# Performance work log

Hardware: AMD Instinct MI355X
Metric: run time of the kernel (lower is better)

The kernel has to match this reference:

```python
import jax, jax.numpy as jnp
import numpy as np

OUT_H, OUT_W = 14, 14
SPATIAL_SCALE = 0.25

def setup_inputs() -> dict:
    key = jax.random.key(0)
    k1, k2, k3, k4, k5, k6 = jax.random.split(key, 6)
    B, C, H, W = 2, 256, 200, 336
    R = 1000
    features = jax.random.normal(k1, (B, C, H, W), jnp.float32)
    img_h, img_w = H / SPATIAL_SCALE, W / SPATIAL_SCALE
    cx = jax.random.uniform(k2, (R,)) * img_w
    cy = jax.random.uniform(k3, (R,)) * img_h
    bw = jax.random.uniform(k4, (R,)) * 256.0 + 16.0
    bh = jax.random.uniform(k5, (R,)) * 256.0 + 16.0
    x1 = jnp.clip(cx - bw / 2, 0.0, img_w - 1.0)
    x2 = jnp.clip(cx + bw / 2, 0.0, img_w - 1.0)
    y1 = jnp.clip(cy - bh / 2, 0.0, img_h - 1.0)
    y2 = jnp.clip(cy + bh / 2, 0.0, img_h - 1.0)
    bidx = jax.random.randint(k6, (R,), 0, B).astype(jnp.float32)
    rois = jnp.stack([bidx, x1, y1, x2, y2], axis=1)  # (R, 5)
    return {"features": features, "rois": rois}

def _roi_align(features, rois):
    # features: (B, C, H, W); rois: (R, 5) = (batch_idx, x1, y1, x2, y2) in image coords
    B, C, H, W = features.shape
    R = rois.shape[0]
    b = jax.lax.stop_gradient(rois[:, 0]).astype(jnp.int32)
    x1, y1, x2, y2 = rois[:, 1], rois[:, 2], rois[:, 3], rois[:, 4]
    # bin-center grid in [0,1] (affine_grid identity, align_corners=False, then normalized)
    gx = (jnp.arange(OUT_W, dtype=features.dtype) + 0.5) / OUT_W
    gy = (jnp.arange(OUT_H, dtype=features.dtype) + 0.5) / OUT_H
    px = x1[:, None] + gx[None, :] * (x2 - x1)[:, None]  # (R, OUT_W) abs image x
    py = y1[:, None] + gy[None, :] * (y2 - y1)[:, None]  # (R, OUT_H) abs image y
    # grid_sample(align_corners=False) with normalized coord abs/(size/scale): pix = abs*scale - 0.5
    fx = jnp.broadcast_to(px[:, None, :], (R, OUT_H, OUT_W)) * SPATIAL_SCALE - 0.5
    fy = jnp.broadcast_to(py[:, :, None], (R, OUT_H, OUT_W)) * SPATIAL_SCALE - 0.5
    x0 = jnp.floor(fx); y0 = jnp.floor(fy)
    lx = fx - x0; ly = fy - y0
    x0i = x0.astype(jnp.int32); y0i = y0.astype(jnp.int32)
    feats_flat = features.reshape(B, C, H * W)
    bb = b[:, None, None]  # (R,1,1)
    def corner(yi, xi):
        valid = ((xi >= 0) & (xi < W) & (yi >= 0) & (yi < H)).astype(features.dtype)
        idx = jnp.clip(yi, 0, H - 1) * W + jnp.clip(xi, 0, W - 1)  # (R,OUT_H,OUT_W)
        v = feats_flat[bb, :, idx]  # (R, OUT_H, OUT_W, C)
        return v * valid[..., None]  # zeros padding_mode
    v00 = corner(y0i, x0i)
    v01 = corner(y0i, x0i + 1)
    v10 = corner(y0i + 1, x0i)
    v11 = corner(y0i + 1, x0i + 1)
    wx0 = (1.0 - lx)[..., None]; wx1 = lx[..., None]
    wy0 = (1.0 - ly)[..., None]; wy1 = ly[..., None]
    out = wy0 * (wx0 * v00 + wx1 * v01) + wy1 * (wx0 * v10 + wx1 * v11)
    return out.transpose(0, 3, 1, 2)  # (R, C, OUT_H, OUT_W)

def reference(features, rois):
    return _roi_align(features, rois)
```

## Files before the change

kernel.cpp:

```cpp
#include <hip/hip_runtime.h>

constexpr int B = 2, C = 256, H = 200, W = 336;
constexpr int HW = H * W;
constexpr int OH = 14, OW = 14, OHW = OH * OW;
constexpr float SCALE = 0.25f;
constexpr int R = 1000;

constexpr int CSPLIT = 16;
constexpr int CPB = C / CSPLIT;
constexpr int NXCD = 8;
constexpr int RPX = R / NXCD;

constexpr int ITEMS = CPB * OHW;

constexpr int NYB = 13;
constexpr int NXB = 21;

typedef float f2 __attribute__((ext_vector_type(2), aligned(4)));

__global__ __launch_bounds__(1024) void bucket_rois_kernel(
    const float* __restrict__ rois, int* __restrict__ order)
{
    __shared__ int cnt[1024];
    const int t = threadIdx.x;
    cnt[t] = 0;
    __syncthreads();

    int k = 0, pos = 0;
    if (t < R) {
        const float* roi = rois + t * 5;
        const int   b  = (int)roi[0];
        const float cx = 0.5f * (roi[1] + roi[3]);
        const float cy = 0.5f * (roi[2] + roi[4]);
        const int yb = min(NYB - 1, max(0, (int)cy >> 6));
        const int xb = min(NXB - 1, max(0, (int)cx >> 6));
        k = (b * NYB + yb) * NXB + xb;
        pos = atomicAdd(&cnt[k], 1);
    }
    __syncthreads();

    for (int off = 1; off < 1024; off <<= 1) {
        const int add = (t >= off) ? cnt[t - off] : 0;
        __syncthreads();
        cnt[t] += add;
        __syncthreads();
    }

    if (t < R) {
        const int base = (k > 0) ? cnt[k - 1] : 0;
        order[base + pos] = t;
    }
}

__global__ __launch_bounds__(256, 8) void roi_align_kernel(
    const float* __restrict__ feat,
    const float* __restrict__ rois,
    const int*  __restrict__ order,
    float* __restrict__ out)
{
    __shared__ int   si0[OHW], si1[OHW];
    __shared__ float sa0[OHW], sb0[OHW], sa1[OHW], sb1[OHW];

    const int bid   = blockIdx.x;
    const int xcd   = bid & (NXCD - 1);
    const int slot  = bid >> 3;
    const int slice = slot & (CSPLIT - 1);
    const int rank  = slot >> 4;
    const int r     = __builtin_amdgcn_readfirstlane(order[xcd * RPX + rank]);
    const int c0    = slice * CPB;
    const int tid   = threadIdx.x;

    const float* roi = rois + r * 5;
    const float x1 = roi[1], y1 = roi[2], x2 = roi[3], y2 = roi[4];
    const int b = __builtin_amdgcn_readfirstlane((int)roi[0]);

    if (tid < OHW) {
        const int oh = tid / OW;
        const int ow = tid - oh * OW;

        const float fx = (x1 + (ow + 0.5f) * (1.0f / OW) * (x2 - x1)) * SCALE - 0.5f;
        const float fy = (y1 + (oh + 0.5f) * (1.0f / OH) * (y2 - y1)) * SCALE - 0.5f;

        const float x0f = floorf(fx), y0f = floorf(fy);
        const float lx = fx - x0f,   ly = fy - y0f;
        const int x0 = (int)x0f,  y0 = (int)y0f;
        const int x1i = x0 + 1,   y1i = y0 + 1;

        const float cxw0 = ((x0  >= 0 && x0  < W) ? 1.0f : 0.0f) * (1.0f - lx);
        const float cxw1 = ((x1i >= 0 && x1i < W) ? 1.0f : 0.0f) * lx;
        const float ryw0 = ((y0  >= 0 && y0  < H) ? 1.0f : 0.0f) * (1.0f - ly);
        const float ryw1 = ((y1i >= 0 && y1i < H) ? 1.0f : 0.0f) * ly;

        const int px = min(max(x0, 0), W - 2);
        const bool swp = (x0 != px);
        const float wxa = swp ? cxw1 : cxw0;
        const float wxb = swp ? cxw0 : cxw1;

        const int cy0 = min(max(y0,  0), H - 1);
        const int cy1 = min(max(y1i, 0), H - 1);

        si0[tid] = cy0 * W + px;
        si1[tid] = cy1 * W + px;
        sa0[tid] = ryw0 * wxa;
        sb0[tid] = ryw0 * wxb;
        sa1[tid] = ryw1 * wxa;
        sb1[tid] = ryw1 * wxb;
    }
    __syncthreads();

    const float* p  = feat + (size_t)(b * C + c0) * HW;
    float*       ob = out  + ((size_t)r * C + c0) * OHW;

    int idx = tid;
    #pragma unroll 1
    for (int bb = 0; bb < 3; ++bb) {
        const float* pa[4];
        const float* pb[4];
        float wa0[4], wb0[4], wa1[4], wb1[4];
        f2 v0[4], v1[4];

        #pragma unroll
        for (int u = 0; u < 4; ++u) {
            const int id = idx + u * 256;
            const int c  = id / OHW;
            const int s  = id - c * OHW;
            const int cb = c * HW;
            pa[u] = p + cb + si0[s];
            pb[u] = p + cb + si1[s];
            wa0[u] = sa0[s]; wb0[u] = sb0[s];
            wa1[u] = sa1[s]; wb1[u] = sb1[s];
        }
        #pragma unroll
        for (int u = 0; u < 4; ++u) {
            v0[u] = *reinterpret_cast<const f2*>(pa[u]);
            v1[u] = *reinterpret_cast<const f2*>(pb[u]);
        }
        __builtin_amdgcn_sched_barrier(0);
        #pragma unroll
        for (int u = 0; u < 4; ++u) {
            const float v = fmaf(wa0[u], v0[u].x,
                            fmaf(wb0[u], v0[u].y,
                            fmaf(wa1[u], v1[u].x, wb1[u] * v1[u].y)));
            __builtin_nontemporal_store(v, ob + idx + u * 256);
        }
        idx += 1024;
    }
    if (idx < ITEMS) {
        const int c  = idx / OHW;
        const int s  = idx - c * OHW;
        const int cb = c * HW;
        const f2 r0 = *reinterpret_cast<const f2*>(p + cb + si0[s]);
        const f2 r1 = *reinterpret_cast<const f2*>(p + cb + si1[s]);
        const float v = fmaf(sa0[s], r0.x,
                        fmaf(sb0[s], r0.y,
                        fmaf(sa1[s], r1.x, sb1[s] * r1.y)));
        __builtin_nontemporal_store(v, ob + idx);
    }
}

extern "C" void kernel_launch(void* const* d_in, const int* in_sizes, int n_in,
                              void* d_out, int out_size, void* d_ws, size_t ws_size,
                              hipStream_t stream) {
    const float* feat = (const float*)d_in[0];
    const float* rois = (const float*)d_in[1];
    float* out = (float*)d_out;
    int* order = (int*)d_ws;

    bucket_rois_kernel<<<1, 1024, 0, stream>>>(rois, order);

    dim3 grid(R * CSPLIT);
    dim3 block(256);
    roi_align_kernel<<<grid, block, 0, stream>>>(feat, rois, order, out);
}
```

Baseline: 383.8 us.

## Software-pipeline gather loads with inline asm and packed LDS tables

Replaces the serial three-iteration gather loop with a double-buffered schedule. It issues the loads for the next batch of eight dwordx2 gathers before consuming the current batch, and places explicit vmcnt waits between stages. Loads are written as inline asm using an SGPR base plus 32-bit VGPR offsets, which cuts 64-bit address arithmetic. The LDS index and weight tables are packed into int2/float4 so each lookup is a single vector read. The cost is higher register pressure from two live load buffers, and the hand-written waitcnt depends on the compiler emitting no other vector memory ops between the waits.

```diff
diff --git a/kernel.cpp b/kernel.cpp
--- a/kernel.cpp
+++ b/kernel.cpp
@@ -16,7 +16,8 @@
 constexpr int NYB = 13;
 constexpr int NXB = 21;
 
-typedef float f2 __attribute__((ext_vector_type(2), aligned(4)));
+typedef float fv2 __attribute__((ext_vector_type(2)));
+typedef float f2u __attribute__((ext_vector_type(2), aligned(4)));
 
 __global__ __launch_bounds__(1024) void bucket_rois_kernel(
     const float* __restrict__ rois, int* __restrict__ order)
@@ -52,14 +53,61 @@
     }
 }
 
+template<int BI>
+__device__ __forceinline__ void issue4(const int tid, const float* p,
+                                       const int2* sidx,
+                                       fv2 (&V0)[4], fv2 (&V1)[4], int (&SS)[4])
+{
+    unsigned o0[4], o1[4];
+    #pragma unroll
+    for (int u = 0; u < 4; ++u) {
+        const int id = tid + (BI * 4 + u) * 256;
+        const int c  = id / OHW;
+        const int s  = id - c * OHW;
+        SS[u] = s;
+        const int2 ii = sidx[s];
+        const unsigned cb4 = (unsigned)c * (unsigned)(HW * 4);
+        o0[u] = cb4 + (unsigned)ii.x * 4u;
+        o1[u] = cb4 + (unsigned)ii.y * 4u;
+    }
+    #pragma unroll
+    for (int u = 0; u < 4; ++u) {
+        asm volatile("global_load_dwordx2 %0, %1, %2"
+                     : "=v"(V0[u]) : "v"(o0[u]), "s"(p) : "memory");
+        asm volatile("global_load_dwordx2 %0, %1, %2"
+                     : "=v"(V1[u]) : "v"(o1[u]), "s"(p) : "memory");
+    }
+}
+
+template<int BI>
+__device__ __forceinline__ void consume4(const int tid, float* ob,
+                                         const float4* sw,
+                                         const fv2 (&V0)[4], const fv2 (&V1)[4],
+                                         const int (&SS)[4])
+{
+    #pragma unroll
+    for (int u = 0; u < 4; ++u) {
+        const float4 w = sw[SS[u]];
+        const float v = fmaf(w.x, V0[u].x,
+                        fmaf(w.y, V0[u].y,
+                        fmaf(w.z, V1[u].x, w.w * V1[u].y)));
+        __builtin_nontemporal_store(v, ob + tid + (BI * 4 + u) * 256);
+    }
+}
+
+#define WAITV(N) do { \
+    asm volatile("s_waitcnt vmcnt(" #N ")" ::: "memory"); \
+    __builtin_amdgcn_sched_barrier(0); \
+} while (0)
+
 __global__ __launch_bounds__(256, 8) void roi_align_kernel(
     const float* __restrict__ feat,
     const float* __restrict__ rois,
     const int*  __restrict__ order,
     float* __restrict__ out)
 {
-    __shared__ int   si0[OHW], si1[OHW];
-    __shared__ float sa0[OHW], sb0[OHW], sa1[OHW], sb1[OHW];
+    __shared__ int2   sidx[OHW];
+    __shared__ float4 sw[OHW];
 
     const int bid   = blockIdx.x;
     const int xcd   = bid & (NXCD - 1);
@@ -99,61 +147,39 @@
         const int cy0 = min(max(y0,  0), H - 1);
         const int cy1 = min(max(y1i, 0), H - 1);
 
-        si0[tid] = cy0 * W + px;
-        si1[tid] = cy1 * W + px;
-        sa0[tid] = ryw0 * wxa;
-        sb0[tid] = ryw0 * wxb;
-        sa1[tid] = ryw1 * wxa;
-        sb1[tid] = ryw1 * wxb;
+        sidx[tid] = make_int2(cy0 * W + px, cy1 * W + px);
+        sw[tid]   = make_float4(ryw0 * wxa, ryw0 * wxb, ryw1 * wxa, ryw1 * wxb);
     }
     __syncthreads();
 
     const float* p  = feat + (size_t)(b * C + c0) * HW;
     float*       ob = out  + ((size_t)r * C + c0) * OHW;
 
-    int idx = tid;
-    #pragma unroll 1
-    for (int bb = 0; bb < 3; ++bb) {
-        const float* pa[4];
-        const float* pb[4];
-        float wa0[4], wb0[4], wa1[4], wb1[4];
-        f2 v0[4], v1[4];
-
-        #pragma unroll
-        for (int u = 0; u < 4; ++u) {
-            const int id = idx + u * 256;
-            const int c  = id / OHW;
-            const int s  = id - c * OHW;
-            const int cb = c * HW;
-            pa[u] = p + cb + si0[s];
-            pb[u] = p + cb + si1[s];
-            wa0[u] = sa0[s]; wb0[u] = sb0[s];
-            wa1[u] = sa1[s]; wb1[u] = sb1[s];
-        }
-        #pragma unroll
-        for (int u = 0; u < 4; ++u) {
-            v0[u] = *reinterpret_cast<const f2*>(pa[u]);
-            v1[u] = *reinterpret_cast<const f2*>(pb[u]);
-        }
-        __builtin_amdgcn_sched_barrier(0);
-        #pragma unroll
-        for (int u = 0; u < 4; ++u) {
-            const float v = fmaf(wa0[u], v0[u].x,
-                            fmaf(wb0[u], v0[u].y,
-                            fmaf(wa1[u], v1[u].x, wb1[u] * v1[u].y)));
-            __builtin_nontemporal_store(v, ob + idx + u * 256);
-        }
-        idx += 1024;
-    }
-    if (idx < ITEMS) {
+    fv2 xa[4], xb[4]; int xs[4];
+    fv2 ya[4], yb[4]; int ys[4];
+
+    issue4<0>(tid, p, sidx, xa, xb, xs);
+    issue4<1>(tid, p, sidx, ya, yb, ys);
+    WAITV(8);
+    consume4<0>(tid, ob, sw, xa, xb, xs);
+    issue4<2>(tid, p, sidx, xa, xb, xs);
+    WAITV(8);
+    consume4<1>(tid, ob, sw, ya, yb, ys);
+    WAITV(0);
+    consume4<2>(tid, ob, sw, xa, xb, xs);
+
+    if (tid < 64) {
+        const int idx = 3072 + tid;
         const int c  = idx / OHW;
         const int s  = idx - c * OHW;
         const int cb = c * HW;
-        const f2 r0 = *reinterpret_cast<const f2*>(p + cb + si0[s]);
-        const f2 r1 = *reinterpret_cast<const f2*>(p + cb + si1[s]);
-        const float v = fmaf(sa0[s], r0.x,
-                        fmaf(sb0[s], r0.y,
-                        fmaf(sa1[s], r1.x, sb1[s] * r1.y)));
+        const int2  ii = sidx[s];
+        const float4 w = sw[s];
+        const f2u r0 = *reinterpret_cast<const f2u*>(p + cb + ii.x);
+        const f2u r1 = *reinterpret_cast<const f2u*>(p + cb + ii.y);
+        const float v = fmaf(w.x, r0.x,
+                        fmaf(w.y, r0.y,
+                        fmaf(w.z, r1.x, w.w * r1.y)));
         __builtin_nontemporal_store(v, ob + idx);
     }
 }
```

Result: no change. 381.1 us (-0.7%).
